# Optimization experiments

Measured on AMD Instinct MI355X. Metric: run time of the kernel, lower is better.

The kernel has to match this reference:

```python
import jax, jax.numpy as jnp
import numpy as np

HEADS = 8

def setup_inputs() -> dict:
    key = jax.random.key(0)
    ks = jax.random.split(key, 5)
    B, C, H, W = 2, 256, 64, 64
    dim = C
    x = jax.random.normal(ks[0], (B, C, H, W), dtype=jnp.float32)
    # Linear weights stored as [in, out] so y = x @ W + b
    w_qkv = jax.random.normal(ks[1], (dim, 3 * dim), dtype=jnp.float32) * (dim ** -0.5)
    b_qkv = jax.random.normal(ks[2], (3 * dim,), dtype=jnp.float32) * 0.02
    w_out = jax.random.normal(ks[3], (dim, dim), dtype=jnp.float32) * (dim ** -0.5)
    b_out = jax.random.normal(ks[4], (dim,), dtype=jnp.float32) * 0.02
    return {"x": x, "w_qkv": w_qkv, "b_qkv": b_qkv, "w_out": w_out, "b_out": b_out}

def reference(x, w_qkv, b_qkv, w_out, b_out):
    B, C, H, W = x.shape
    h = HEADS
    d = C // h
    scale = d ** -0.5
    # [B, C, H, W] -> [B, N, C]
    tokens = x.reshape(B, C, H * W).transpose(0, 2, 1)
    qkv = tokens @ w_qkv + b_qkv  # [B, N, 3C]
    q, k, v = jnp.split(qkv, 3, axis=-1)
    def to_heads(t):
        Bn, N, _ = t.shape
        return t.reshape(Bn, N, h, d).transpose(0, 2, 1, 3)  # [B, h, N, d]
    q, k, v = map(to_heads, (q, k, v))
    dots = jnp.einsum('bhnd,bhmd->bhnm', q, k) * scale  # [B, h, N, N]
    attn = jax.nn.softmax(dots, axis=-1)
    out = jnp.einsum('bhnm,bhmd->bhnd', attn, v)  # [B, h, N, d]
    out = out.transpose(0, 2, 1, 3).reshape(B, H * W, C)  # [B, N, C]
    out = out @ w_out + b_out
    return out.transpose(0, 2, 1).reshape(B, C, H, W)
```

## Files before the change

kernel.cpp:

```cpp
#include <hip/hip_runtime.h>

typedef __attribute__((ext_vector_type(8))) short s16x8;
typedef __attribute__((ext_vector_type(4))) float f32x4;
typedef __attribute__((ext_vector_type(16))) float f32x16;
typedef __attribute__((ext_vector_type(2))) unsigned u32x2;
typedef __attribute__((ext_vector_type(4))) unsigned u32x4;

#define MFMA32(a, b, c) __builtin_amdgcn_mfma_f32_16x16x32_bf16((a), (b), (c), 0, 0, 0)

#if __has_builtin(__builtin_amdgcn_mfma_f32_32x32x16_bf16)
#define MFMA3216(a, b, c) __builtin_amdgcn_mfma_f32_32x32x16_bf16((a), (b), (c), 0, 0, 0)
#else
#define MFMA3216(a, b, c) (c)
#endif

#if __has_builtin(__builtin_amdgcn_exp2f)
#define EXP2F(x) __builtin_amdgcn_exp2f(x)
#else
#define EXP2F(x) __exp2f(x)
#endif

#if __has_builtin(__builtin_amdgcn_rcpf)
#define RCPF(x) __builtin_amdgcn_rcpf(x)
#else
#define RCPF(x) (1.0f / (x))
#endif

#define SL2E 0.25507313f

__device__ __forceinline__ unsigned pkrne(float a, float b) {
  unsigned ua = __builtin_bit_cast(unsigned, a);
  unsigned ub = __builtin_bit_cast(unsigned, b);
  ua += 0x7FFFu + ((ua >> 16) & 1u);
  ub += 0x7FFFu + ((ub >> 16) & 1u);
  return __builtin_amdgcn_perm(ub, ua, 0x07060302u);
}

__device__ __forceinline__ unsigned pktrunc(float a, float b) {
  return __builtin_amdgcn_perm(__builtin_bit_cast(unsigned, b),
                               __builtin_bit_cast(unsigned, a), 0x07060302u);
}

__device__ __forceinline__ unsigned short bfr(float f) {
  unsigned u = __builtin_bit_cast(unsigned, f);
  u += 0x7FFFu + ((u >> 16) & 1u);
  return (unsigned short)(u >> 16);
}

__device__ __forceinline__ float bflo(unsigned u) {
  return __builtin_bit_cast(float, u << 16);
}
__device__ __forceinline__ float bfhi(unsigned u) {
  return __builtin_bit_cast(float, u & 0xFFFF0000u);
}

__device__ __forceinline__ u32x2 plswap(unsigned a, unsigned b) {
#if __has_builtin(__builtin_amdgcn_permlane32_swap)
  return __builtin_amdgcn_permlane32_swap(a, b, false, false);
#else
  unsigned sa = (unsigned)__shfl_xor((int)a, 32, 64);
  unsigned sb = (unsigned)__shfl_xor((int)b, 32, 64);
  bool hi = (threadIdx.x & 63) >= 32;
  u32x2 r;
  r.x = hi ? sb : a;
  r.y = hi ? b : sa;
  return r;
#endif
}

__device__ __forceinline__ void stage16(const ushort* g, ushort* l, int lane) {
#if __has_builtin(__builtin_amdgcn_global_load_lds)
  __builtin_amdgcn_global_load_lds(
      (__attribute__((address_space(1))) unsigned int*)(unsigned long long)(
          const void*)g,
      (__attribute__((address_space(3))) unsigned int*)(unsigned)(
          unsigned long long)(const void*)l,
      16, 0, 0);
#else
  *(uint4*)(l + lane * 8) = *(const uint4*)g;
#endif
}

__global__ __launch_bounds__(256) void prep_kernel(
    const float* __restrict__ x, const float* __restrict__ wqkv,
    const float* __restrict__ wout, ushort* __restrict__ xbf,
    ushort* __restrict__ wT, ushort* __restrict__ woT) {
  const int t = threadIdx.x;
  const int sub = t & 15, grp = t >> 4;
  const int id = blockIdx.x;
  const float* src;
  ushort* dst;
  int src_ld, k0, n0;
  float sc = 1.f;
  if (id < 512) {
    int mt = id & 63, kt = (id >> 6) & 3, b = id >> 8;
    src = x + (size_t)b * 256 * 4096;
    src_ld = 4096;
    dst = xbf + (size_t)b * 4096 * 256;
    k0 = kt * 64;
    n0 = mt * 64;
  } else if (id < 560) {
    int r = id - 512, nt = r % 12, kt = r / 12;
    src = wqkv;
    src_ld = 768;
    dst = wT;
    k0 = kt * 64;
    n0 = nt * 64;
    if (n0 < 256) sc = SL2E;
  } else {
    int r = id - 560, nt = r & 3, kt = r >> 2;
    src = wout;
    src_ld = 256;
    dst = woT;
    k0 = kt * 64;
    n0 = nt * 64;
  }
  const int k = k0 + grp * 4;
  const int n = n0 + sub * 4;
  unsigned d0[4], d1[4];
#pragma unroll
  for (int i = 0; i < 4; ++i) {
    float4 v = *(const float4*)(src + (size_t)(k + i) * src_ld + n);
    d0[i] = pkrne(v.x * sc, v.y * sc);
    d1[i] = pkrne(v.z * sc, v.w * sc);
  }
  u32x2 r0 = {__builtin_amdgcn_perm(d0[1], d0[0], 0x05040100u),
              __builtin_amdgcn_perm(d0[3], d0[2], 0x05040100u)};
  u32x2 r1 = {__builtin_amdgcn_perm(d0[1], d0[0], 0x07060302u),
              __builtin_amdgcn_perm(d0[3], d0[2], 0x07060302u)};
  u32x2 r2 = {__builtin_amdgcn_perm(d1[1], d1[0], 0x05040100u),
              __builtin_amdgcn_perm(d1[3], d1[2], 0x05040100u)};
  u32x2 r3 = {__builtin_amdgcn_perm(d1[1], d1[0], 0x07060302u),
              __builtin_amdgcn_perm(d1[3], d1[2], 0x07060302u)};
  *(u32x2*)(dst + (size_t)(n + 0) * 256 + k) = r0;
  *(u32x2*)(dst + (size_t)(n + 1) * 256 + k) = r1;
  *(u32x2*)(dst + (size_t)(n + 2) * 256 + k) = r2;
  *(u32x2*)(dst + (size_t)(n + 3) * 256 + k) = r3;
}

__global__ __launch_bounds__(256) void qkv_kernel(
    const ushort* __restrict__ xbf, const ushort* __restrict__ wT,
    const float* __restrict__ bq, ushort* __restrict__ QG,
    ushort* __restrict__ KG, ushort* __restrict__ VtG) {
  __shared__ __align__(16) ushort Wl[64][40];
  __shared__ __align__(16) ushort Xl[128][40];
  const int t0 = blockIdx.x * 128;
  const int n0 = blockIdx.y * 64;
  const int t = threadIdx.x;
  const int wid = t >> 6, lane = t & 63;
  const int wy = wid >> 1, wx = wid & 1;
  const int quad = lane >> 4, l16 = lane & 15;
  f32x4 acc[2][4] = {};
  const int wr = t >> 2, wsg = t & 3;
  for (int k0 = 0; k0 < 256; k0 += 32) {
    __syncthreads();
    *(uint4*)&Wl[wr][wsg * 8] =
        *(const uint4*)(wT + (size_t)(n0 + wr) * 256 + k0 + wsg * 8);
#pragma unroll
    for (int i = 0; i < 2; ++i) {
      int fid = t + 256 * i, row = fid >> 2, seg = fid & 3;
      *(uint4*)&Xl[row][seg * 8] =
          *(const uint4*)(xbf + (size_t)(t0 + row) * 256 + k0 + seg * 8);
    }
    __syncthreads();
    s16x8 wf[2], xf[4];
#pragma unroll
    for (int i = 0; i < 2; ++i)
      wf[i] = *(const s16x8*)&Wl[32 * wy + 16 * i + l16][quad * 8];
#pragma unroll
    for (int j = 0; j < 4; ++j)
      xf[j] = *(const s16x8*)&Xl[64 * wx + 16 * j + l16][quad * 8];
#pragma unroll
    for (int i = 0; i < 2; ++i)
#pragma unroll
      for (int j = 0; j < 4; ++j) acc[i][j] = MFMA32(wf[i], xf[j], acc[i][j]);
  }
  if (n0 < 512) {
    ushort* dst = (n0 < 256) ? QG : KG;
    const float bsc = (n0 < 256) ? SL2E : 1.f;
#pragma unroll
    for (int i = 0; i < 2; ++i) {
      int nb = n0 + 32 * wy + 16 * i + 4 * quad;
      float4 b4 = *(const float4*)(bq + nb);
      float bx0 = b4.x * bsc, bx1 = b4.y * bsc, bx2 = b4.z * bsc,
            bx3 = b4.w * bsc;
      int h = ((nb & 255) >> 5);
      int dd0 = nb & 31;
#pragma unroll
      for (int j = 0; j < 4; ++j) {
        int tok = t0 + 64 * wx + 16 * j + l16;
        int b = tok >> 12, tokn = tok & 4095;
        u32x2 pk = {pkrne(acc[i][j][0] + bx0, acc[i][j][1] + bx1),
                    pkrne(acc[i][j][2] + bx2, acc[i][j][3] + bx3)};
        *(u32x2*)(dst + ((size_t)(b * 8 + h) * 4096 + tokn) * 32 + dd0) = pk;
      }
    }
  } else {
#pragma unroll
    for (int i = 0; i < 2; ++i) {
      int nb = n0 + 32 * wy + 16 * i + 4 * quad;
      float4 b4 = *(const float4*)(bq + nb);
      float bb[4] = {b4.x, b4.y, b4.z, b4.w};
#pragma unroll
      for (int r = 0; r < 4; ++r) {
        int nn = nb + r - 512;
        int h = nn >> 5, ddv = nn & 31;
        ushort* vrow = VtG + (size_t)(h * 32 + ddv) * 4096;
#pragma unroll
        for (int j = 0; j < 4; ++j) {
          int tok = t0 + 64 * wx + 16 * j + l16;
          int b = tok >> 12, tokn = tok & 4095;
          vrow[(size_t)b * 8 * 32 * 4096 + tokn] = bfr(acc[i][j][r] + bb[r]);
        }
      }
    }
  }
}

__global__ __launch_bounds__(256, 4) void attn_split(
    const ushort* __restrict__ QG, const ushort* __restrict__ KG,
    const ushort* __restrict__ VtG, ushort* __restrict__ OF0,
    ushort* __restrict__ OFb, float* __restrict__ LF) {
  __shared__ __align__(64) ushort KVs[2][4096];
  const int id = blockIdx.x;
  const int bh = (id & 7) * 2 + ((id >> 3) & 1);
  const int q0 = ((id >> 4) & 31) * 128;
  const int sp = id >> 9;
  const int kt0 = (sp * 64 + 2) / 3;
  const int niter = ((sp + 1) * 64 + 2) / 3 - kt0;
  const int t = threadIdx.x;
  const int wid = t >> 6, lane = t & 63;
  const int l5 = lane & 31, hi = lane >> 5;
  const size_t base = (size_t)bh * 4096 * 32;
  const ushort* qp = QG + base;
  const ushort* kp = KG + base;
  const ushort* vp = VtG + base;
  const int qw = q0 + 32 * wid;
  const ushort* qrow = qp + (size_t)(qw + l5) * 32 + hi * 8;
  const s16x8 qf0 = *(const s16x8*)(qrow);
  const s16x8 qf1 = *(const s16x8*)(qrow + 16);
  const int sK = wid >> 1, hK = wid & 1;
  const int kdst = sK * 1024 + hK * 512;
  const ushort* kpre =
      kp + (size_t)(kt0 * 64 + sK * 32 + l5) * 32 + hK * 16 + hi * 8;
  const ushort* vpre =
      vp + (size_t)l5 * 4096 + kt0 * 64 + sK * 32 + hK * 16 + hi * 8;
  stage16(kpre, &KVs[0][kdst], lane);
  stage16(vpre, &KVs[0][2048 + kdst], lane);
  kpre += 2048;
  vpre += 64;
  __syncthreads();
  f32x16 o = {};
  float lacc = 0.f;
  for (int i = 0; i < niter; ++i) {
    const int cur = i & 1;
    if (i + 1 < niter) {
      stage16(kpre, &KVs[cur ^ 1][kdst], lane);
      stage16(vpre, &KVs[cur ^ 1][2048 + kdst], lane);
      kpre += 2048;
      vpre += 64;
    }
    const ushort* kb = &KVs[cur][0];
    const ushort* vb = &KVs[cur][2048];
#pragma unroll
    for (int s = 0; s < 2; ++s) {
      const s16x8 ka0 = *(const s16x8*)(kb + s * 1024 + lane * 8);
      const s16x8 ka1 = *(const s16x8*)(kb + s * 1024 + 512 + lane * 8);
      f32x16 S = {};
      S = MFMA3216(ka0, qf0, S);
      S = MFMA3216(ka1, qf1, S);
      unsigned w8[8];
#pragma unroll
      for (int ii = 0; ii < 8; ++ii)
        w8[ii] = pktrunc(EXP2F(S[2 * ii]), EXP2F(S[2 * ii + 1]));
#pragma unroll
      for (int ii = 0; ii < 8; ++ii) lacc += bflo(w8[ii]) + bfhi(w8[ii]);
      u32x2 sw0 = plswap(w8[0], w8[2]);
      u32x2 sw1 = plswap(w8[1], w8[3]);
      u32x2 sw2 = plswap(w8[4], w8[6]);
      u32x2 sw3 = plswap(w8[5], w8[7]);
      u32x4 pa0 = {sw0.x, sw1.x, sw0.y, sw1.y};
      u32x4 pa1 = {sw2.x, sw3.x, sw2.y, sw3.y};
      const s16x8 va0 = *(const s16x8*)(vb + s * 1024 + lane * 8);
      const s16x8 va1 = *(const s16x8*)(vb + s * 1024 + 512 + lane * 8);
      o = MFMA3216(__builtin_bit_cast(s16x8, pa0), va0, o);
      o = MFMA3216(__builtin_bit_cast(s16x8, pa1), va1, o);
    }
    __syncthreads();
  }
  ushort* OFs = (sp == 0) ? OF0 : OFb + (size_t)(sp - 1) * 2097152;
  float* LFs = LF + (size_t)sp * 65536;
#pragma unroll
  for (int r = 0; r < 16; ++r) {
    int q = qw + (r & 3) + 8 * (r >> 2) + 4 * hi;
    OFs[((size_t)bh * 4096 + q) * 32 + l5] = bfr(o[r]);
  }
  float lw = lacc + __shfl_xor(lacc, 32, 64);
  if (lane < 32) LFs[(size_t)bh * 4096 + qw + lane] = lw;
}

__global__ __launch_bounds__(256) void proj_split(
    const ushort* __restrict__ OF0, const ushort* __restrict__ OFb,
    const float* __restrict__ LF, const ushort* __restrict__ woT,
    const float* __restrict__ bo, float* __restrict__ out) {
  __shared__ __align__(16) ushort Wl[64][40];
  __shared__ __align__(16) ushort Xl[128][40];
  const int t0 = blockIdx.x * 128;
  const int c0 = blockIdx.y * 64;
  const int t = threadIdx.x;
  const int wid = t >> 6, lane = t & 63;
  const int wy = wid >> 1, wx = wid & 1;
  const int quad = lane >> 4, l16 = lane & 15;
  f32x4 acc[2][4] = {};
  const int wr = t >> 2, wsg = t & 3;
  const int c8 = (t & 7) * 4;
  for (int k0 = 0; k0 < 256; k0 += 32) {
    __syncthreads();
    *(uint4*)&Wl[wr][wsg * 8] =
        *(const uint4*)(woT + (size_t)(c0 + wr) * 256 + k0 + wsg * 8);
    const int hh = k0 >> 5;
#pragma unroll
    for (int p = 0; p < 4; ++p) {
      int row = 32 * p + (t >> 3);
      int tok = t0 + row, bb = tok >> 12, tokn = tok & 4095;
      size_t ro = (size_t)(bb * 8 + hh) * 4096 + tokn;
      size_t oi = ro * 32 + c8;
      uint2 a0 = *(const uint2*)(OF0 + oi);
      uint2 a1 = *(const uint2*)(OFb + oi);
      uint2 a2 = *(const uint2*)(OFb + 2097152 + oi);
      float l = LF[ro] + LF[65536 + ro] + LF[131072 + ro];
      float inv = RCPF(l);
      f32x4 s;
      s[0] = bflo(a0.x) + bflo(a1.x) + bflo(a2.x);
      s[1] = bfhi(a0.x) + bfhi(a1.x) + bfhi(a2.x);
      s[2] = bflo(a0.y) + bflo(a1.y) + bflo(a2.y);
      s[3] = bfhi(a0.y) + bfhi(a1.y) + bfhi(a2.y);
      s *= inv;
      u32x2 pk = {pkrne(s[0], s[1]), pkrne(s[2], s[3])};
      *(u32x2*)&Xl[row][c8] = pk;
    }
    __syncthreads();
    s16x8 wf[2], xf[4];
#pragma unroll
    for (int i = 0; i < 2; ++i)
      wf[i] = *(const s16x8*)&Wl[32 * wy + 16 * i + l16][quad * 8];
#pragma unroll
    for (int j = 0; j < 4; ++j)
      xf[j] = *(const s16x8*)&Xl[64 * wx + 16 * j + l16][quad * 8];
#pragma unroll
    for (int i = 0; i < 2; ++i)
#pragma unroll
      for (int j = 0; j < 4; ++j) acc[i][j] = MFMA32(wf[i], xf[j], acc[i][j]);
  }
#pragma unroll
  for (int i = 0; i < 2; ++i) {
    int cb = c0 + 32 * wy + 16 * i + 4 * quad;
    float4 b4 = *(const float4*)(bo + cb);
    float bb[4] = {b4.x, b4.y, b4.z, b4.w};
#pragma unroll
    for (int j = 0; j < 4; ++j) {
      int tok = t0 + 64 * wx + 16 * j + l16;
      int b = tok >> 12, tokn = tok & 4095;
#pragma unroll
      for (int r = 0; r < 4; ++r)
        out[((size_t)(b * 256 + cb + r)) * 4096 + tokn] = acc[i][j][r] + bb[r];
    }
  }
}

extern "C" void kernel_launch(void* const* d_in, const int* in_sizes, int n_in,
                              void* d_out, int out_size, void* d_ws, size_t ws_size,
                              hipStream_t stream) {
  (void)in_sizes; (void)n_in; (void)out_size; (void)ws_size;
  const float* x = (const float*)d_in[0];
  const float* wq = (const float*)d_in[1];
  const float* bq = (const float*)d_in[2];
  const float* wo = (const float*)d_in[3];
  const float* bo = (const float*)d_in[4];
  float* out = (float*)d_out;
  ushort* ws = (ushort*)d_ws;
  ushort* xbf = ws;
  ushort* OF0 = ws;
  ushort* QG  = ws + 2097152;
  ushort* KG  = ws + 4194304;
  ushort* VtG = ws + 6291456;
  ushort* wT  = ws + 8388608;
  ushort* woT = ws + 8585216;
  ushort* OFb = ws + 8650752;
  float* LF = (float*)(ws + 12845056);
  prep_kernel<<<576, 256, 0, stream>>>(x, wq, wo, xbf, wT, woT);
  qkv_kernel<<<dim3(64, 12), 256, 0, stream>>>(xbf, wT, bq, QG, KG, VtG);
  attn_split<<<1536, 256, 0, stream>>>(QG, KG, VtG, OF0, OFb, LF);
  proj_split<<<dim3(64, 4), 256, 0, stream>>>(OF0, OFb, LF, woT, bo, out);
}
```

Baseline: 146.0 us.

## Use two-way key split in attention and compute row sums with MFMA

```diff
diff --git a/kernel.cpp b/kernel.cpp
--- a/kernel.cpp
+++ b/kernel.cpp
@@ -226,8 +226,8 @@
   const int bh = (id & 7) * 2 + ((id >> 3) & 1);
   const int q0 = ((id >> 4) & 31) * 128;
   const int sp = id >> 9;
-  const int kt0 = (sp * 64 + 2) / 3;
-  const int niter = ((sp + 1) * 64 + 2) / 3 - kt0;
+  const int kt0 = sp * 32;
+  const int niter = 32;
   const int t = threadIdx.x;
   const int wid = t >> 6, lane = t & 63;
   const int l5 = lane & 31, hi = lane >> 5;
@@ -251,7 +251,10 @@
   vpre += 64;
   __syncthreads();
   f32x16 o = {};
-  float lacc = 0.f;
+  f32x16 o_l = {};
+  const s16x8 ones8 = {(short)0x3F80, (short)0x3F80, (short)0x3F80,
+                       (short)0x3F80, (short)0x3F80, (short)0x3F80,
+                       (short)0x3F80, (short)0x3F80};
   for (int i = 0; i < niter; ++i) {
     const int cur = i & 1;
     if (i + 1 < niter) {
@@ -273,30 +276,35 @@
 #pragma unroll
       for (int ii = 0; ii < 8; ++ii)
         w8[ii] = pktrunc(EXP2F(S[2 * ii]), EXP2F(S[2 * ii + 1]));
-#pragma unroll
-      for (int ii = 0; ii < 8; ++ii) lacc += bflo(w8[ii]) + bfhi(w8[ii]);
       u32x2 sw0 = plswap(w8[0], w8[2]);
       u32x2 sw1 = plswap(w8[1], w8[3]);
       u32x2 sw2 = plswap(w8[4], w8[6]);
       u32x2 sw3 = plswap(w8[5], w8[7]);
       u32x4 pa0 = {sw0.x, sw1.x, sw0.y, sw1.y};
       u32x4 pa1 = {sw2.x, sw3.x, sw2.y, sw3.y};
+      const s16x8 pA0 = __builtin_bit_cast(s16x8, pa0);
+      const s16x8 pA1 = __builtin_bit_cast(s16x8, pa1);
       const s16x8 va0 = *(const s16x8*)(vb + s * 1024 + lane * 8);
       const s16x8 va1 = *(const s16x8*)(vb + s * 1024 + 512 + lane * 8);
-      o = MFMA3216(__builtin_bit_cast(s16x8, pa0), va0, o);
-      o = MFMA3216(__builtin_bit_cast(s16x8, pa1), va1, o);
+      o = MFMA3216(pA0, va0, o);
+      o = MFMA3216(pA1, va1, o);
+      o_l = MFMA3216(pA0, ones8, o_l);
+      o_l = MFMA3216(pA1, ones8, o_l);
     }
     __syncthreads();
   }
-  ushort* OFs = (sp == 0) ? OF0 : OFb + (size_t)(sp - 1) * 2097152;
+  ushort* OFs = (sp == 0) ? OF0 : OFb;
   float* LFs = LF + (size_t)sp * 65536;
 #pragma unroll
   for (int r = 0; r < 16; ++r) {
     int q = qw + (r & 3) + 8 * (r >> 2) + 4 * hi;
     OFs[((size_t)bh * 4096 + q) * 32 + l5] = bfr(o[r]);
   }
-  float lw = lacc + __shfl_xor(lacc, 32, 64);
-  if (lane < 32) LFs[(size_t)bh * 4096 + qw + lane] = lw;
+  float lval = o_l[0];
+#pragma unroll
+  for (int r = 1; r < 16; ++r) lval = (l5 == r) ? o_l[r] : lval;
+  if (l5 < 16)
+    LFs[(size_t)bh * 4096 + qw + (l5 & 3) + 8 * (l5 >> 2) + 4 * hi] = lval;
 }
 
 __global__ __launch_bounds__(256) void proj_split(
@@ -327,14 +335,13 @@
       size_t oi = ro * 32 + c8;
       uint2 a0 = *(const uint2*)(OF0 + oi);
       uint2 a1 = *(const uint2*)(OFb + oi);
-      uint2 a2 = *(const uint2*)(OFb + 2097152 + oi);
-      float l = LF[ro] + LF[65536 + ro] + LF[131072 + ro];
+      float l = LF[ro] + LF[65536 + ro];
       float inv = RCPF(l);
       f32x4 s;
-      s[0] = bflo(a0.x) + bflo(a1.x) + bflo(a2.x);
-      s[1] = bfhi(a0.x) + bfhi(a1.x) + bfhi(a2.x);
-      s[2] = bflo(a0.y) + bflo(a1.y) + bflo(a2.y);
-      s[3] = bfhi(a0.y) + bfhi(a1.y) + bfhi(a2.y);
+      s[0] = bflo(a0.x) + bflo(a1.x);
+      s[1] = bfhi(a0.x) + bfhi(a1.x);
+      s[2] = bflo(a0.y) + bflo(a1.y);
+      s[3] = bfhi(a0.y) + bfhi(a1.y);
       s *= inv;
       u32x2 pk = {pkrne(s[0], s[1]), pkrne(s[2], s[3])};
       *(u32x2*)&Xl[row][c8] = pk;
@@ -390,6 +397,6 @@
   float* LF = (float*)(ws + 12845056);
   prep_kernel<<<576, 256, 0, stream>>>(x, wq, wo, xbf, wT, woT);
   qkv_kernel<<<dim3(64, 12), 256, 0, stream>>>(xbf, wT, bq, QG, KG, VtG);
-  attn_split<<<1536, 256, 0, stream>>>(QG, KG, VtG, OF0, OFb, LF);
+  attn_split<<<1024, 256, 0, stream>>>(QG, KG, VtG, OF0, OFb, LF);
   proj_split<<<dim3(64, 4), 256, 0, stream>>>(OF0, OFb, LF, woT, bo, out);
 }
```

New measurement: 139.7 us. 4.3% less time.
